# Optimization experiments

Measured on AMD Instinct MI355X. Metric: run time of the kernel, lower is better.

Reference implementation:

```python
import jax, jax.numpy as jnp
import numpy as np
import math

IN_F, OUT_F, GRID = 1024, 1024, 7
BATCH, SEQ = 4, 4096


def _l2norm(v, eps=1e-12):
    return v / (jnp.linalg.norm(v) + eps)


def setup_inputs() -> dict:
    key = jax.random.key(0)
    k0, k1, k2, k3 = jax.random.split(key, 4)
    x = jax.random.normal(k0, (BATCH, SEQ, IN_F), dtype=jnp.float32)
    # spectral-normed base linear (weights nonzero for a meaningful baseline)
    base_w = jax.random.normal(k1, (OUT_F, IN_F), dtype=jnp.float32) * 0.02
    base_b = jnp.zeros((OUT_F,), dtype=jnp.float32)
    u = jax.random.normal(k2, (OUT_F,), dtype=jnp.float32)  # power-iteration buffer
    # Chebyshev translation points and fixed logspace scales (as in __init__)
    steps = jnp.arange(GRID, dtype=jnp.float32)
    translation = (-jnp.cos((2.0 * steps + 1.0) / (2.0 * GRID) * math.pi) * 1.5).reshape(1, 1, GRID)
    scale = (1.0 * jnp.logspace(-0.5, 0.5, GRID)).reshape(1, 1, GRID).astype(jnp.float32)
    wavelet_w = jax.random.normal(k3, (OUT_F, IN_F * GRID), dtype=jnp.float32) * 0.01
    soft_threshold = jnp.array([0.005], dtype=jnp.float32)
    output_scale = jnp.array([1.0], dtype=jnp.float32)
    return dict(x=x, base_w=base_w, base_b=base_b, u=u, translation=translation,
                scale=scale, wavelet_w=wavelet_w, soft_threshold=soft_threshold,
                output_scale=output_scale)


def reference(x, base_w, base_b, u, translation, scale, wavelet_w, soft_threshold, output_scale):
    x_flat = x.reshape(-1, x.shape[-1])  # [N, IN]
    # spectral norm: one power iteration (no grad through u, v), sigma = u' W v
    v = jax.lax.stop_gradient(_l2norm(base_w.T @ u))
    u2 = jax.lax.stop_gradient(_l2norm(base_w @ v))
    sigma = u2 @ (base_w @ v)
    w_sn = base_w / sigma
    base_out = jax.nn.silu(x_flat) @ w_sn.T + base_b  # [N, OUT]
    # wavelet (Ricker) basis expansion
    safe_scale = jnp.maximum(jnp.abs(scale), 0.1)  # [1,1,G]
    x_norm = jnp.tanh(x_flat) * 2.5  # [N, IN]
    xe = (x_norm[:, :, None] - translation) / safe_scale  # [N, IN, G]
    basis = (1.0 - xe * xe) * jnp.exp(-0.5 * xe * xe)
    kan = basis.reshape(x_flat.shape[0], -1) @ wavelet_w.T  # [N, OUT]
    thr = jax.nn.softplus(soft_threshold)
    kan = jnp.sign(kan) * jax.nn.relu(jnp.abs(kan) - thr)
    out = (base_out + kan) * output_scale
    return out.reshape(*x.shape[:-1], wavelet_w.shape[0])
```

## Files before the change

kernel.cpp:

```cpp
#include <hip/hip_runtime.h>
#include <math.h>


typedef __attribute__((ext_vector_type(4))) float  f32x4;
typedef __attribute__((ext_vector_type(8))) __bf16 bf16x8;
typedef __attribute__((ext_vector_type(8))) unsigned short u16x8;

#define NROWS 16384
#define INF   1024
#define OUTF  1024
#define GG    7
#define KKAN  7168
#define KTOT  8192

static __device__ __forceinline__ unsigned short f2bf(float f) {
  union { float f; unsigned int u; } v; v.f = f;
  unsigned int r = v.u + 0x7fffu + ((v.u >> 16) & 1u);
  return (unsigned short)(r >> 16);
}

__global__ void mv_wt_u(const float* __restrict__ W, const float* __restrict__ u,
                        float* __restrict__ t) {
  int j = blockIdx.x;
  int tid = threadIdx.x;
  float p = 0.f;
  for (int i = tid; i < OUTF; i += 256) p += W[(size_t)i * INF + j] * u[i];
  __shared__ float red[256];
  red[tid] = p; __syncthreads();
  for (int s = 128; s > 0; s >>= 1) { if (tid < s) red[tid] += red[tid + s]; __syncthreads(); }
  if (tid == 0) t[j] = red[0];
}

__global__ void mv_w_t(const float* __restrict__ W, const float* __restrict__ t,
                       float* __restrict__ s) {
  int i = blockIdx.x;
  int tid = threadIdx.x;
  float p = 0.f;
  for (int j = tid; j < INF; j += 256) p += W[(size_t)i * INF + j] * t[j];
  __shared__ float red[256];
  red[tid] = p; __syncthreads();
  for (int k = 128; k > 0; k >>= 1) { if (tid < k) red[tid] += red[tid + k]; __syncthreads(); }
  if (tid == 0) s[i] = red[0];
}

__global__ void sigma_finish(const float* __restrict__ t, const float* __restrict__ s,
                             const float* __restrict__ st, const float* __restrict__ os,
                             float* __restrict__ scal) {
  __shared__ float r1[256], r2[256];
  int tid = threadIdx.x;
  float p1 = 0.f, p2 = 0.f;
  for (int i = tid; i < 1024; i += 256) { float a = t[i]; p1 += a * a; float b = s[i]; p2 += b * b; }
  r1[tid] = p1; r2[tid] = p2; __syncthreads();
  for (int k = 128; k > 0; k >>= 1) { if (tid < k) { r1[tid] += r1[tid + k]; r2[tid] += r2[tid + k]; } __syncthreads(); }
  if (tid == 0) {
    float nt = sqrtf(r1[0]);
    float ns = sqrtf(r2[0]);
    float nq = ns / (nt + 1e-12f);
    float sigma = nq * nq / (nq + 1e-12f);
    scal[0] = 1.f / sigma;
    scal[1] = log1pf(__expf(st[0]));
    scal[2] = os[0];
  }
}

__global__ void wsn_cast(const float* __restrict__ w, const float* __restrict__ scal,
                         unsigned short* __restrict__ Wp) {
  float is = scal[0];
  int idx = blockIdx.x * 256 + threadIdx.x;
  int row = idx >> 7, i0 = (idx & 127) << 3;
  const f32x4* p = (const f32x4*)(w + (size_t)row * INF + i0);
  f32x4 a = p[0], b = p[1];
  u16x8 v;
  v[0] = f2bf(a[0] * is); v[1] = f2bf(a[1] * is); v[2] = f2bf(a[2] * is); v[3] = f2bf(a[3] * is);
  v[4] = f2bf(b[0] * is); v[5] = f2bf(b[1] * is); v[6] = f2bf(b[2] * is); v[7] = f2bf(b[3] * is);
  *(u16x8*)(Wp + (size_t)row * KTOT + KKAN + i0) = v;
}

__global__ void wkan_cast(const float* __restrict__ w, unsigned short* __restrict__ Wp) {
  __shared__ float row[KKAN];
  int orow = blockIdx.x;
  const float* src = w + (size_t)orow * KKAN;
  for (int c = threadIdx.x * 4; c < KKAN; c += 1024)
    *(f32x4*)&row[c] = *(const f32x4*)&src[c];
  __syncthreads();
  unsigned short* dst = Wp + (size_t)orow * KTOT;
  for (int r = threadIdx.x; r < 896; r += 256) {
    int g = r >> 7, i0 = (r & 127) << 3;
    u16x8 v;
#pragma unroll
    for (int j = 0; j < 8; j++) v[j] = f2bf(row[(i0 + j) * GG + g]);
    *(u16x8*)(dst + g * 1024 + i0) = v;
  }
}

__global__ void expand_kernel(const float* __restrict__ x,
                              const float* __restrict__ translation,
                              const float* __restrict__ scale,
                              unsigned short* __restrict__ Ap,
                              int row0, int nrows) {
  float tr[GG], iss[GG];
#pragma unroll
  for (int g = 0; g < GG; g++) {
    tr[g] = translation[g];
    float s = fabsf(scale[g]);
    iss[g] = 1.f / (s < 0.1f ? 0.1f : s);
  }
  int units = nrows * (INF / 8);
  int stride = gridDim.x * blockDim.x;
  for (int uu = blockIdx.x * blockDim.x + threadIdx.x; uu < units; uu += stride) {
    int nloc = uu >> 7;
    int i0 = (uu & 127) << 3;
    const f32x4* xp = (const f32x4*)(x + (size_t)(row0 + nloc) * INF + i0);
    f32x4 xa = xp[0], xb = xp[1];
    float xv[8] = {xa[0], xa[1], xa[2], xa[3], xb[0], xb[1], xb[2], xb[3]};
    u16x8 sb, kb[GG];
#pragma unroll
    for (int j = 0; j < 8; j++) {
      float xx = xv[j];
      float si = xx / (1.f + __expf(-xx));
      sb[j] = f2bf(si);
      float e2 = __expf(2.f * xx);
      float xn = 2.5f * (1.f - 2.f / (e2 + 1.f));
#pragma unroll
      for (int g = 0; g < GG; g++) {
        float xe = (xn - tr[g]) * iss[g];
        float t2 = xe * xe;
        float b = (1.f - t2) * __expf(-0.5f * t2);
        kb[g][j] = f2bf(b);
      }
    }
    unsigned short* rp = Ap + (size_t)nloc * KTOT;
    *(u16x8*)(rp + KKAN + i0) = sb;
#pragma unroll
    for (int g = 0; g < GG; g++) *(u16x8*)(rp + g * 1024 + i0) = kb[g];
  }
}

static __device__ __forceinline__ void gload16(const unsigned short* g, unsigned short* l) {
  __builtin_amdgcn_global_load_lds(
      (const __attribute__((address_space(1))) unsigned int*)g,
      (__attribute__((address_space(3))) unsigned int*)l, 16, 0, 0);
}

#define SBAR  do { __builtin_amdgcn_sched_barrier(0); __builtin_amdgcn_s_barrier(); } while (0)
#define LGKM0 do { asm volatile("s_waitcnt lgkmcnt(0)" ::: "memory"); __builtin_amdgcn_sched_barrier(0); } while (0)
#define VM(N) asm volatile("s_waitcnt vmcnt(" #N ")" ::: "memory")

#define STAGE_A(bb, hh, tt) do { \
    const unsigned short* _s = gA + (size_t)((hh) * 128) * KTOT + (size_t)(tt) * 64; \
    unsigned short* _d = ldA + (bb) * 16384 + (hh) * 8192; \
    gload16(_s, _d); \
    gload16(_s + (size_t)64 * KTOT, _d + 4096); \
  } while (0)

#define STAGE_B(bb, tt) do { \
    const unsigned short* _s = gB + (size_t)(tt) * 64; \
    unsigned short* _d = ldB + (bb) * 8192; \
    gload16(_s, _d); \
    gload16(_s + (size_t)64 * KTOT, _d + 4096); \
  } while (0)

#define RD_A(bb, kx) do { _Pragma("unroll") for (int i = 0; i < 4; ++i) \
    af[i] = *(const bf16x8*)(pA + (bb) * 32768 + i * 2048 + (kx)); } while (0)

#define RD_B(bb, jg, kx) do { _Pragma("unroll") for (int jj = 0; jj < 2; ++jj) \
    bf[jj] = *(const bf16x8*)(pB + (bb) * 16384 + ((jg) * 2 + jj) * 2048 + (kx)); } while (0)

#define MMp(jg) do { _Pragma("unroll") for (int i = 0; i < 4; ++i) \
    _Pragma("unroll") for (int jj = 0; jj < 2; ++jj) \
      acc[i][(jg) * 2 + jj] = __builtin_amdgcn_mfma_f32_16x16x32_bf16(af[i], bf[jj], acc[i][(jg) * 2 + jj], 0, 0, 0); } while (0)

#define TILE(tt, bb, SB, SA, WAIT) do { \
    RD_A(bb, kx0); RD_B(bb, 0, kx0); \
    if (SB) STAGE_B((bb) ^ 1, (tt) + 1); \
    SBAR; LGKM0; \
    __builtin_amdgcn_s_setprio(1); MMp(0); __builtin_amdgcn_s_setprio(0); \
    SBAR; \
    RD_B(bb, 1, kx0); \
    SBAR; LGKM0; \
    __builtin_amdgcn_s_setprio(1); MMp(1); __builtin_amdgcn_s_setprio(0); \
    SBAR; \
    RD_A(bb, kx1); RD_B(bb, 0, kx1); \
    SBAR; LGKM0; \
    __builtin_amdgcn_s_setprio(1); MMp(0); __builtin_amdgcn_s_setprio(0); \
    SBAR; \
    RD_B(bb, 1, kx1); \
    if (SA) { STAGE_A(bb, 0, (tt) + 2); STAGE_A(bb, 1, (tt) + 2); } \
    SBAR; LGKM0; \
    __builtin_amdgcn_s_setprio(1); MMp(1); __builtin_amdgcn_s_setprio(0); \
    WAIT; \
    SBAR; \
  } while (0)

__global__ __launch_bounds__(512, 2) void gemm_k(
    const unsigned short* __restrict__ A,
    const unsigned short* __restrict__ W,
    const float* __restrict__ bias,
    const float* __restrict__ scal,
    float* __restrict__ out) {
  __shared__ unsigned short lds[49152];

  int bid = blockIdx.x;
  int cpx = gridDim.x >> 3;
  int swz = (bid & 7) * cpx + (bid >> 3);
  int m0 = (swz >> 3) * 256;
  int n0 = (swz & 7) * 128;
  int tid = threadIdx.x;
  int wv = tid >> 6, l = tid & 63;
  int wr = wv >> 1, wc = wv & 1;

  float thr = scal[1], osc = scal[2];

  int rowq = tid >> 3;
  int swk = ((tid & 7) ^ (rowq & 7)) << 3;
  const unsigned short* gA = A + (size_t)(m0 + rowq) * KTOT + swk;
  const unsigned short* gB = W + (size_t)(n0 + rowq) * KTOT + swk;
  unsigned short* ldA = lds + wv * 512;
  unsigned short* ldB = lds + 32768 + wv * 512;

  int lr = l & 15;
  int kx0 = (((l >> 4) << 4) ^ ((l & 7) << 4));
  int kx1 = kx0 ^ 64;
  const char* pA = (const char*)lds + (wr * 64 + lr) * 128;
  const char* pB = (const char*)lds + 65536 + (wc * 64 + lr) * 128;

  bf16x8 af[4], bf[2];
  f32x4 acc[4][4] = {};

  STAGE_A(0, 0, 0);
  STAGE_A(0, 1, 0);
  STAGE_B(0, 0);
  STAGE_A(1, 0, 1);
  STAGE_A(1, 1, 1);
  VM(4);
  SBAR;

  for (int t = 0; t < 112; t += 2) {
    TILE(t,     0, 1, 1, VM(4));
    TILE(t + 1, 1, 1, 1, VM(4));
  }

#pragma unroll
  for (int i = 0; i < 4; ++i)
#pragma unroll
    for (int j = 0; j < 4; ++j)
#pragma unroll
      for (int e = 0; e < 4; ++e) {
        float v = acc[i][j][e];
        float a = fabsf(v) - thr;
        a = a > 0.f ? a : 0.f;
        acc[i][j][e] = v > 0.f ? a : -a;
      }

  for (int t = 112; t < 126; t += 2) {
    TILE(t,     0, 1, 1, VM(4));
    TILE(t + 1, 1, 1, 1, VM(4));
  }
  TILE(126, 0, 1, 0, VM(0));
  TILE(127, 1, 0, 0, (void)0);

  int rr = m0 + wr * 64 + ((l >> 4) << 2);
  int cc = n0 + wc * 64 + lr;
#pragma unroll
  for (int i = 0; i < 4; ++i)
#pragma unroll
    for (int j = 0; j < 4; ++j) {
      int c = cc + j * 16;
      float bc = bias[c];
#pragma unroll
      for (int e = 0; e < 4; ++e) {
        int r = rr + i * 16 + e;
        out[(size_t)r * OUTF + c] = (acc[i][j][e] + bc) * osc;
      }
    }
}

extern "C" void kernel_launch(void* const* d_in, const int* in_sizes, int n_in,
                              void* d_out, int out_size, void* d_ws, size_t ws_size,
                              hipStream_t stream) {
  const float* x              = (const float*)d_in[0];
  const float* base_w         = (const float*)d_in[1];
  const float* base_b         = (const float*)d_in[2];
  const float* u              = (const float*)d_in[3];
  const float* translation    = (const float*)d_in[4];
  const float* scale          = (const float*)d_in[5];
  const float* wavelet_w      = (const float*)d_in[6];
  const float* soft_threshold = (const float*)d_in[7];
  const float* output_scale   = (const float*)d_in[8];
  float* out = (float*)d_out;

  char* ws = (char*)d_ws;
  float* t_vec = (float*)ws;
  float* s_vec = t_vec + 1024;
  float* scal  = s_vec + 1024;
  unsigned short* Wp = (unsigned short*)(ws + 16384);
  char* dynbuf = ws + 16384 + (size_t)KTOT * OUTF * 2;

  size_t fixed = 16384 + (size_t)KTOT * OUTF * 2;
  size_t avail = ws_size > fixed ? ws_size - fixed : 0;

  mv_wt_u<<<1024, 256, 0, stream>>>(base_w, u, t_vec);
  mv_w_t<<<1024, 256, 0, stream>>>(base_w, t_vec, s_vec);
  sigma_finish<<<1, 256, 0, stream>>>(t_vec, s_vec, soft_threshold, output_scale, scal);
  wsn_cast<<<512, 256, 0, stream>>>(base_w, scal, Wp);
  wkan_cast<<<1024, 256, 0, stream>>>(wavelet_w, Wp);

  const size_t ROW = (size_t)KTOT * 2;
  size_t total = (size_t)NROWS * ROW;
  int nch = (int)((total + (avail > 0 ? avail : 1) - 1) / (avail > 0 ? avail : 1));
  if (nch < 1) nch = 1;
  long mc = (((NROWS + nch - 1) / nch) + 255) & ~255L;
  while (mc > 256 && (size_t)mc * ROW > avail) mc -= 256;
  if (mc < 256) mc = 256;

  unsigned short* Ap = (unsigned short*)dynbuf;

  for (long r0 = 0; r0 < NROWS; r0 += mc) {
    long nr = (NROWS - r0 < mc) ? (NROWS - r0) : mc;
    expand_kernel<<<2048, 256, 0, stream>>>(x, translation, scale, Ap, (int)r0, (int)nr);
    int mt = (int)(nr / 256);
    gemm_k<<<mt * 8, 512, 0, stream>>>(Ap, Wp, base_b, scal, out + (size_t)r0 * OUTF);
  }
}
```

Before: 363.1 us.

## Switch GEMM main loop to triple-buffered LDS with one barrier per tile

The bf16 GEMM pipeline moves from double buffering (A and B staged at different points) to a three-stage LDS ring, where A and B are staged together two tiles ahead. Each tile now loads all A and B fragments for both k-halves up front and issues 32 MFMAs, separated only by lgkmcnt waits, with a single workgroup barrier per tile instead of eight. This aims to cut barrier and synchronization overhead and hide more global-load latency. In exchange LDS use rises to 144KB per block, which may limit occupancy under launch_bounds(512,2), and more fragment registers are live at once.

```diff
diff --git a/kernel.cpp b/kernel.cpp
--- a/kernel.cpp
+++ b/kernel.cpp
@@ -142,52 +142,45 @@
       (__attribute__((address_space(3))) unsigned int*)l, 16, 0, 0);
 }
 
-#define SBAR  do { __builtin_amdgcn_sched_barrier(0); __builtin_amdgcn_s_barrier(); } while (0)
-#define LGKM0 do { asm volatile("s_waitcnt lgkmcnt(0)" ::: "memory"); __builtin_amdgcn_sched_barrier(0); } while (0)
+#define SCB   __builtin_amdgcn_sched_barrier(0)
+#define SBAR  do { SCB; __builtin_amdgcn_s_barrier(); } while (0)
 #define VM(N) asm volatile("s_waitcnt vmcnt(" #N ")" ::: "memory")
-
-#define STAGE_A(bb, hh, tt) do { \
-    const unsigned short* _s = gA + (size_t)((hh) * 128) * KTOT + (size_t)(tt) * 64; \
-    unsigned short* _d = ldA + (bb) * 16384 + (hh) * 8192; \
-    gload16(_s, _d); \
-    gload16(_s + (size_t)64 * KTOT, _d + 4096); \
+#define LG(N) asm volatile("s_waitcnt lgkmcnt(" #N ")" ::: "memory")
+
+#define STAGE(db, tt) do { \
+    const unsigned short* _sa = gA + (size_t)(tt) * 64; \
+    const unsigned short* _sb = gB + (size_t)(tt) * 64; \
+    unsigned short* _da = ldsS + (db) * 24576; \
+    unsigned short* _db = ldsS + (db) * 24576 + 16384; \
+    gload16(_sa,                       _da); \
+    gload16(_sa + (size_t)64  * KTOT,  _da + 4096); \
+    gload16(_sa + (size_t)128 * KTOT,  _da + 8192); \
+    gload16(_sa + (size_t)192 * KTOT,  _da + 12288); \
+    gload16(_sb,                       _db); \
+    gload16(_sb + (size_t)64  * KTOT,  _db + 4096); \
   } while (0)
 
-#define STAGE_B(bb, tt) do { \
-    const unsigned short* _s = gB + (size_t)(tt) * 64; \
-    unsigned short* _d = ldB + (bb) * 8192; \
-    gload16(_s, _d); \
-    gload16(_s + (size_t)64 * KTOT, _d + 4096); \
-  } while (0)
-
-#define RD_A(bb, kx) do { _Pragma("unroll") for (int i = 0; i < 4; ++i) \
-    af[i] = *(const bf16x8*)(pA + (bb) * 32768 + i * 2048 + (kx)); } while (0)
-
-#define RD_B(bb, jg, kx) do { _Pragma("unroll") for (int jj = 0; jj < 2; ++jj) \
-    bf[jj] = *(const bf16x8*)(pB + (bb) * 16384 + ((jg) * 2 + jj) * 2048 + (kx)); } while (0)
-
-#define MMp(jg) do { _Pragma("unroll") for (int i = 0; i < 4; ++i) \
-    _Pragma("unroll") for (int jj = 0; jj < 2; ++jj) \
-      acc[i][(jg) * 2 + jj] = __builtin_amdgcn_mfma_f32_16x16x32_bf16(af[i], bf[jj], acc[i][(jg) * 2 + jj], 0, 0, 0); } while (0)
-
-#define TILE(tt, bb, SB, SA, WAIT) do { \
-    RD_A(bb, kx0); RD_B(bb, 0, kx0); \
-    if (SB) STAGE_B((bb) ^ 1, (tt) + 1); \
-    SBAR; LGKM0; \
-    __builtin_amdgcn_s_setprio(1); MMp(0); __builtin_amdgcn_s_setprio(0); \
-    SBAR; \
-    RD_B(bb, 1, kx0); \
-    SBAR; LGKM0; \
-    __builtin_amdgcn_s_setprio(1); MMp(1); __builtin_amdgcn_s_setprio(0); \
-    SBAR; \
-    RD_A(bb, kx1); RD_B(bb, 0, kx1); \
-    SBAR; LGKM0; \
-    __builtin_amdgcn_s_setprio(1); MMp(0); __builtin_amdgcn_s_setprio(0); \
-    SBAR; \
-    RD_B(bb, 1, kx1); \
-    if (SA) { STAGE_A(bb, 0, (tt) + 2); STAGE_A(bb, 1, (tt) + 2); } \
-    SBAR; LGKM0; \
-    __builtin_amdgcn_s_setprio(1); MMp(1); __builtin_amdgcn_s_setprio(0); \
+#define RD_A(dst, bb, kx) do { _Pragma("unroll") for (int i = 0; i < 4; ++i) \
+    dst[i] = *(const bf16x8*)(pA + (bb) * 49152 + i * 2048 + (kx)); } while (0)
+
+#define RD_B(dst, bb, kx) do { _Pragma("unroll") for (int j = 0; j < 4; ++j) \
+    dst[j] = *(const bf16x8*)(pB + (bb) * 49152 + j * 2048 + (kx)); } while (0)
+
+#define MM16(AF, BF) do { _Pragma("unroll") for (int i = 0; i < 4; ++i) \
+    _Pragma("unroll") for (int j = 0; j < 4; ++j) \
+      acc[i][j] = __builtin_amdgcn_mfma_f32_16x16x32_bf16(AF[i], BF[j], acc[i][j], 0, 0, 0); } while (0)
+
+#define TILE(tt, bb, db, SS, WAIT) do { \
+    RD_A(af0, bb, kx0); RD_B(bf0r, bb, kx0); \
+    SCB; \
+    RD_A(af1, bb, kx1); RD_B(bf1r, bb, kx1); \
+    SCB; \
+    if (SS) STAGE(db, (tt) + 2); \
+    SCB; \
+    LG(8); SCB; \
+    __builtin_amdgcn_s_setprio(1); MM16(af0, bf0r); __builtin_amdgcn_s_setprio(0); \
+    LG(0); SCB; \
+    __builtin_amdgcn_s_setprio(1); MM16(af1, bf1r); __builtin_amdgcn_s_setprio(0); \
     WAIT; \
     SBAR; \
   } while (0)
@@ -198,7 +191,7 @@
     const float* __restrict__ bias,
     const float* __restrict__ scal,
     float* __restrict__ out) {
-  __shared__ unsigned short lds[49152];
+  __shared__ unsigned short lds[73728];
 
   int bid = blockIdx.x;
   int cpx = gridDim.x >> 3;
@@ -215,30 +208,31 @@
   int swk = ((tid & 7) ^ (rowq & 7)) << 3;
   const unsigned short* gA = A + (size_t)(m0 + rowq) * KTOT + swk;
   const unsigned short* gB = W + (size_t)(n0 + rowq) * KTOT + swk;
-  unsigned short* ldA = lds + wv * 512;
-  unsigned short* ldB = lds + 32768 + wv * 512;
+  unsigned short* ldsS = lds + wv * 512;
 
   int lr = l & 15;
   int kx0 = (((l >> 4) << 4) ^ ((l & 7) << 4));
   int kx1 = kx0 ^ 64;
   const char* pA = (const char*)lds + (wr * 64 + lr) * 128;
-  const char* pB = (const char*)lds + 65536 + (wc * 64 + lr) * 128;
-
-  bf16x8 af[4], bf[2];
+  const char* pB = (const char*)lds + 32768 + (wc * 64 + lr) * 128;
+
+  bf16x8 af0[4], af1[4], bf0r[4], bf1r[4];
   f32x4 acc[4][4] = {};
 
-  STAGE_A(0, 0, 0);
-  STAGE_A(0, 1, 0);
-  STAGE_B(0, 0);
-  STAGE_A(1, 0, 1);
-  STAGE_A(1, 1, 1);
-  VM(4);
+  STAGE(0, 0);
+  STAGE(1, 1);
+  VM(6);
   SBAR;
 
-  for (int t = 0; t < 112; t += 2) {
-    TILE(t,     0, 1, 1, VM(4));
-    TILE(t + 1, 1, 1, 1, VM(4));
-  }
+  for (int t = 0; t < 108; t += 3) {
+    TILE(t,     0, 2, 1, VM(6));
+    TILE(t + 1, 1, 0, 1, VM(6));
+    TILE(t + 2, 2, 1, 1, VM(6));
+  }
+  TILE(108, 0, 2, 1, VM(6));
+  TILE(109, 1, 0, 1, VM(6));
+  TILE(110, 2, 1, 1, VM(6));
+  TILE(111, 0, 2, 1, VM(6));
 
 #pragma unroll
   for (int i = 0; i < 4; ++i)
@@ -252,12 +246,15 @@
         acc[i][j][e] = v > 0.f ? a : -a;
       }
 
-  for (int t = 112; t < 126; t += 2) {
-    TILE(t,     0, 1, 1, VM(4));
-    TILE(t + 1, 1, 1, 1, VM(4));
-  }
-  TILE(126, 0, 1, 0, VM(0));
-  TILE(127, 1, 0, 0, (void)0);
+  for (int t = 112; t < 124; t += 3) {
+    TILE(t,     1, 0, 1, VM(6));
+    TILE(t + 1, 2, 1, 1, VM(6));
+    TILE(t + 2, 0, 2, 1, VM(6));
+  }
+  TILE(124, 1, 0, 1, VM(6));
+  TILE(125, 2, 1, 1, VM(6));
+  TILE(126, 0, 2, 0, VM(0));
+  TILE(127, 1, 2, 0, (void)0);
 
   int rr = m0 + wr * 64 + ((l >> 4) << 2);
   int cc = n0 + wc * 64 + lr;
```

Result: faster. 333.6 us (-8.1%).
